# Kernel tuning notes

Hardware: AMD Instinct MI355X
Metric: run time of the kernel (lower is better)

Reference implementation:

```python
import jax, jax.numpy as jnp
import numpy as np

N = 100000
E = 3200000
B = 8192
IN_DIM = 18   # enc_dim for khops=2
HID = 64
EMB = 32


def setup_inputs() -> dict:
    key = jax.random.key(0)
    ks = jax.random.split(key, 10)
    x = jax.random.normal(ks[0], (N, IN_DIM), dtype=jnp.float32)
    ei = jax.random.randint(ks[1], (2, E), 0, N, dtype=jnp.int64)
    targets = jax.random.randint(ks[2], (2, B), 0, N, dtype=jnp.int64)
    # GCN layer params (glorot-ish scale)
    W1 = jax.random.normal(ks[3], (IN_DIM, HID), dtype=jnp.float32) / np.sqrt(IN_DIM)
    b1 = jnp.zeros((HID,), dtype=jnp.float32)
    W2 = jax.random.normal(ks[4], (HID, EMB), dtype=jnp.float32) / np.sqrt(HID)
    b2 = jnp.zeros((EMB,), dtype=jnp.float32)
    Wo = jax.random.normal(ks[5], (EMB, 1), dtype=jnp.float32) / np.sqrt(EMB)
    bo = jnp.zeros((1,), dtype=jnp.float32)
    return {"x": x, "ei": ei, "targets": targets,
            "W1": W1, "b1": b1, "W2": W2, "b2": b2, "Wo": Wo, "bo": bo}


def _gcn_conv(x, W, b, src, dst, norm, n_nodes):
    # x' = D^{-1/2}(A+I)D^{-1/2} X W + b  (self-loops already in src/dst)
    h = x @ W                                  # [N, F_out]
    msg = h[src] * norm[:, None]               # [E+N, F_out] gather
    agg = jax.ops.segment_sum(msg, dst, num_segments=n_nodes)  # scatter-add
    return agg + b


def reference(x, ei, targets, W1, b1, W2, b2, Wo, bo):
    n = x.shape[0]
    loop = jnp.arange(n, dtype=ei.dtype)
    src = jnp.concatenate([ei[0], loop])
    dst = jnp.concatenate([ei[1], loop])
    deg = jax.ops.segment_sum(jnp.ones_like(src, dtype=x.dtype), dst, num_segments=n)
    dis = jax.lax.rsqrt(deg)                   # deg >= 1 (self-loops)
    norm = dis[src] * dis[dst]
    # 2-layer GCN (khops=2): relu between layers, dropout=0 (eval)
    h = jax.nn.relu(_gcn_conv(x, W1, b1, src, dst, norm, n))
    z = _gcn_conv(h, W2, b2, src, dst, norm, n)
    # node-pair multiply + linear head
    pair = z[targets[0]] * z[targets[1]]       # [B, EMB]
    return pair @ Wo + bo                      # [B, 1]
```

## Files before the change

### kernel.cpp

```cpp
#include <hip/hip_runtime.h>

#define IN_DIM 18
#define XPAD 20
#define HID 64
#define EMB 32
#define NGROUP 8
#define PSHIFT 9
#define PMAX 200
#define BCAP 40
#define TILE 4096
#define SCAP 16896

typedef int vint4 __attribute__((ext_vector_type(4)));
typedef unsigned long long u64;

__device__ inline float4 shfl_f4(float4 v, int srcLane) {
    float4 r;
    r.x = __shfl(v.x, srcLane);
    r.y = __shfl(v.y, srcLane);
    r.z = __shfl(v.z, srcLane);
    r.w = __shfl(v.w, srcLane);
    return r;
}

__device__ inline float4 shfl_xor_f4(float4 v, int m) {
    v.x = __shfl_xor(v.x, m);
    v.y = __shfl_xor(v.y, m);
    v.z = __shfl_xor(v.z, m);
    v.w = __shfl_xor(v.w, m);
    return v;
}


__global__ void k_init(int* __restrict__ deg, int* __restrict__ gcnt, int n) {
    int i = blockIdx.x * 256 + threadIdx.x;
    if (i < n) deg[i] = 1;
    if (i < 256) gcnt[i] = 0;
}


__global__ void k_part(const int* __restrict__ src, const int* __restrict__ dst,
                       int* __restrict__ gcnt, u64* __restrict__ gbuf,
                       int e, int Pp, int cap) {
    __shared__ u64 sbuf[PMAX][BCAP];
    __shared__ int scnt[PMAX];
    __shared__ int sbase[PMAX];
    int tid = threadIdx.x;
    int ntile = (e + TILE - 1) / TILE;
    for (int tile = blockIdx.x; tile < ntile; tile += gridDim.x) {
        for (int p = tid; p < Pp; p += 256) scnt[p] = 0;
        __syncthreads();
#pragma unroll
        for (int r = 0; r < TILE / 1024; ++r) {
            int i = tile * TILE + (r * 256 + tid) * 4;
            if (i + 4 <= e) {
                vint4 s4 = __builtin_nontemporal_load((const vint4*)(src + i));
                vint4 d4 = __builtin_nontemporal_load((const vint4*)(dst + i));
#pragma unroll
                for (int k = 0; k < 4; ++k) {
                    int d = d4[k];
                    int p = d >> PSHIFT;
                    u64 pr = ((u64)(unsigned)s4[k] << 32) | (unsigned)d;
                    int pos = atomicAdd(&scnt[p], 1);
                    if (pos < BCAP) sbuf[p][pos] = pr;
                    else {
                        int gp = atomicAdd(&gcnt[p], 1);
                        __builtin_nontemporal_store(pr, &gbuf[(size_t)p * cap + gp]);
                    }
                }
            } else if (i < e) {
                for (int k = i; k < e; ++k) {
                    int d = dst[k];
                    int p = d >> PSHIFT;
                    u64 pr = ((u64)(unsigned)src[k] << 32) | (unsigned)d;
                    int pos = atomicAdd(&scnt[p], 1);
                    if (pos < BCAP) sbuf[p][pos] = pr;
                    else {
                        int gp = atomicAdd(&gcnt[p], 1);
                        __builtin_nontemporal_store(pr, &gbuf[(size_t)p * cap + gp]);
                    }
                }
            }
        }
        __syncthreads();
        for (int p = tid; p < Pp; p += 256)
            sbase[p] = atomicAdd(&gcnt[p], min(scnt[p], BCAP));
        __syncthreads();
        int wid = tid >> 6, lane = tid & 63;
        for (int p = wid; p < Pp; p += 4) {
            int c = min(scnt[p], BCAP);
            int b = sbase[p];
            for (int k = lane; k < c; k += 64)
                __builtin_nontemporal_store(sbuf[p][k], &gbuf[(size_t)p * cap + b + k]);
        }
        __syncthreads();
    }
}


__global__ void k_gscan(const int* __restrict__ gcnt, int* __restrict__ gbase, int Pp) {
    __shared__ int s[256];
    int t = threadIdx.x;
    int v = (t < Pp) ? gcnt[t] : 0;
    s[t] = v;
    __syncthreads();
    for (int off = 1; off < 256; off <<= 1) {
        int u = (t >= off) ? s[t - off] : 0;
        __syncthreads();
        s[t] += u;
        __syncthreads();
    }
    if (t < Pp) gbase[t] = s[t] - v;
}


__global__ void k_build(const u64* __restrict__ gbuf, const int* __restrict__ gcnt,
                        const int* __restrict__ gbase, int* __restrict__ deg,
                        float* __restrict__ dis, int* __restrict__ row_ptr,
                        int* __restrict__ adj, int cap, int n) {
    __shared__ u64 spairs[SCAP];
    __shared__ int sdeg[512];
    __shared__ int sexcl[512];
    __shared__ int swp[512];
    __shared__ int sscan[512];
    int p = blockIdx.x;
    int tid = threadIdx.x;
    int lo = p << PSHIFT;
    int nn = min(n - lo, 512);
    int cnt = gcnt[p];
    int base = gbase[p];
    const u64* buf = gbuf + (size_t)p * cap;

    sdeg[tid] = 0;
    int scap = min(cnt, SCAP);
    for (int k = tid; k < scap; k += 512)
        spairs[k] = __builtin_nontemporal_load(&buf[k]);
    __syncthreads();
    for (int k = tid; k < cnt; k += 512) {
        u64 pr = (k < SCAP) ? spairs[k] : __builtin_nontemporal_load(&buf[k]);
        atomicAdd(&sdeg[(int)(pr & 0xffffffffu) - lo], 1);
    }
    __syncthreads();
    int v = sdeg[tid];
    sscan[tid] = v;
    __syncthreads();
    for (int off = 1; off < 512; off <<= 1) {
        int u = (tid >= off) ? sscan[tid - off] : 0;
        __syncthreads();
        sscan[tid] += u;
        __syncthreads();
    }
    sexcl[tid] = sscan[tid] - v;
    swp[tid] = 0;
    __syncthreads();
    if (tid < nn) {
        int dg = sdeg[tid] + 1;
        deg[lo + tid] = dg;
        dis[lo + tid] = rsqrtf((float)dg);
        row_ptr[lo + tid] = base + sexcl[tid];
    }
    for (int k = tid; k < cnt; k += 512) {
        u64 pr = (k < SCAP) ? spairs[k] : __builtin_nontemporal_load(&buf[k]);
        int dl = (int)(pr & 0xffffffffu) - lo;
        int slot = sexcl[dl] + atomicAdd(&swp[dl], 1);
        adj[base + slot] = (int)(pr >> 32);
    }
}


__global__ void k_count_part(const int* __restrict__ dst, int* __restrict__ deg,
                             int e, int nrange, int n) {
    int g  = blockIdx.x & (NGROUP - 1);
    int lo = g * nrange;
    int hi = min(n, lo + nrange);
    int bid  = blockIdx.x >> 3;
    int nblk = gridDim.x >> 3;
    int i0   = (bid * 256 + threadIdx.x) * 4;
    int step = nblk * 256 * 4;
    for (int i = i0; i < e; i += step) {
        if (i + 4 <= e) {
            int4 d4 = *(const int4*)(dst + i);
            if (d4.x >= lo && d4.x < hi) atomicAdd(&deg[d4.x], 1);
            if (d4.y >= lo && d4.y < hi) atomicAdd(&deg[d4.y], 1);
            if (d4.z >= lo && d4.z < hi) atomicAdd(&deg[d4.z], 1);
            if (d4.w >= lo && d4.w < hi) atomicAdd(&deg[d4.w], 1);
        } else {
            for (int k = i; k < e; ++k) {
                int d = dst[k];
                if (d >= lo && d < hi) atomicAdd(&deg[d], 1);
            }
        }
    }
}

__global__ void k_dis(const int* __restrict__ deg, float* __restrict__ dis, int n) {
    int i = blockIdx.x * 256 + threadIdx.x;
    if (i < n) dis[i] = rsqrtf((float)deg[i]);
}

__global__ void k_scanA(const int* __restrict__ deg, int* __restrict__ row_ptr,
                        int* __restrict__ blksums, int n) {
    __shared__ int s[1024];
    int tid = threadIdx.x;
    int i = blockIdx.x * 1024 + tid;
    int v = (i < n) ? (deg[i] - 1) : 0;
    s[tid] = v;
    __syncthreads();
    for (int off = 1; off < 1024; off <<= 1) {
        int t = (tid >= off) ? s[tid - off] : 0;
        __syncthreads();
        s[tid] += t;
        __syncthreads();
    }
    if (i < n) row_ptr[i] = s[tid] - v;
    if (tid == 1023) blksums[blockIdx.x] = s[1023];
}

__global__ void k_scanB(const int* __restrict__ blksums, int* __restrict__ blkoffs, int nb) {
    __shared__ int s[1024];
    int tid = threadIdx.x;
    int v = (tid < nb) ? blksums[tid] : 0;
    s[tid] = v;
    __syncthreads();
    for (int off = 1; off < 1024; off <<= 1) {
        int t = (tid >= off) ? s[tid - off] : 0;
        __syncthreads();
        s[tid] += t;
        __syncthreads();
    }
    if (tid < nb) blkoffs[tid] = s[tid] - v;
}

__global__ void k_scanC(int* __restrict__ row_ptr, const int* __restrict__ blkoffs,
                        int* __restrict__ write_ptr, int n) {
    int i = blockIdx.x * 1024 + threadIdx.x;
    if (i < n) {
        int r = row_ptr[i] + blkoffs[blockIdx.x];
        row_ptr[i] = r;
        write_ptr[i] = r;
    }
}

__global__ void k_fill_part(const int* __restrict__ src, const int* __restrict__ dst,
                            int* __restrict__ write_ptr, int* __restrict__ adj,
                            int e, int nrange, int n) {
    int g  = blockIdx.x & (NGROUP - 1);
    int lo = g * nrange;
    int hi = min(n, lo + nrange);
    int bid  = blockIdx.x >> 3;
    int nblk = gridDim.x >> 3;
    int i0   = (bid * 256 + threadIdx.x) * 4;
    int step = nblk * 256 * 4;
    for (int i = i0; i < e; i += step) {
        if (i + 4 <= e) {
            int4 d4 = *(const int4*)(dst + i);
            if (d4.x >= lo && d4.x < hi) { int slot = atomicAdd(&write_ptr[d4.x], 1); adj[slot] = src[i];     }
            if (d4.y >= lo && d4.y < hi) { int slot = atomicAdd(&write_ptr[d4.y], 1); adj[slot] = src[i + 1]; }
            if (d4.z >= lo && d4.z < hi) { int slot = atomicAdd(&write_ptr[d4.z], 1); adj[slot] = src[i + 2]; }
            if (d4.w >= lo && d4.w < hi) { int slot = atomicAdd(&write_ptr[d4.w], 1); adj[slot] = src[i + 3]; }
        } else {
            for (int k = i; k < e; ++k) {
                int d = dst[k];
                if (d >= lo && d < hi) { int slot = atomicAdd(&write_ptr[d], 1); adj[slot] = src[k]; }
            }
        }
    }
}


__global__ void k_xn(const float* __restrict__ x, const float* __restrict__ dis,
                     float* __restrict__ xn, int n) {
    int gid = blockIdx.x * 256 + threadIdx.x;
    if (gid >= n * 5) return;
    int i = gid / 5, s = gid - (gid / 5) * 5;
    float dn = dis[i];
    const float* xr = x + (size_t)i * IN_DIM;
    float4 v;
    int k = s * 4;
    v.x = (k + 0 < IN_DIM) ? xr[k + 0] * dn : 0.f;
    v.y = (k + 1 < IN_DIM) ? xr[k + 1] * dn : 0.f;
    v.z = (k + 2 < IN_DIM) ? xr[k + 2] * dn : 0.f;
    v.w = (k + 3 < IN_DIM) ? xr[k + 3] * dn : 0.f;
    *(float4*)(xn + (size_t)i * XPAD + k) = v;
}


__global__ void k_agg1f(const float* __restrict__ xn, const int* __restrict__ row_ptr,
                        const int* __restrict__ deg, const int* __restrict__ adj,
                        const float* __restrict__ dis, const float* __restrict__ W1,
                        const float* __restrict__ b1, const float* __restrict__ W2,
                        float* __restrict__ hn2, int n) {
    __shared__ float sw[IN_DIM * HID];
    __shared__ float sw2[HID * EMB];
    __shared__ float sb[HID];
    __shared__ __align__(16) float sagg[4][XPAD];
    __shared__ float sh[4][HID];
    int tid = threadIdx.x;
    for (int t = tid; t < IN_DIM * HID; t += 256) sw[t] = W1[t];
    for (int t = tid; t < HID * EMB; t += 256) sw2[t] = W2[t];
    if (tid < HID) sb[tid] = b1[tid];
    __syncthreads();
    int node = blockIdx.x * 4 + (tid >> 6);
    if (node >= n) return;
    int lane = tid & 63;
    int wv = tid >> 6;
    int eg = lane / 5;
    int sl = lane - eg * 5;
    bool act = eg < 12;
    int beg = row_ptr[node];
    int cnt = deg[node] - 1;
    const int* a = adj + beg;
    float4 acc = make_float4(0.f, 0.f, 0.f, 0.f);
    int base = 0;
    for (; base + 24 <= cnt; base += 24) {
        if (act) {
            int j0 = a[base + eg];
            int j1 = a[base + 12 + eg];
            float4 v0 = *(const float4*)(xn + (size_t)j0 * XPAD + sl * 4);
            float4 v1 = *(const float4*)(xn + (size_t)j1 * XPAD + sl * 4);
            acc.x += v0.x + v1.x; acc.y += v0.y + v1.y;
            acc.z += v0.z + v1.z; acc.w += v0.w + v1.w;
        }
    }
    if (act && base + eg < cnt) {
        float4 v = *(const float4*)(xn + (size_t)a[base + eg] * XPAD + sl * 4);
        acc.x += v.x; acc.y += v.y; acc.z += v.z; acc.w += v.w;
    }
    if (act && base + 12 + eg < cnt) {
        float4 v = *(const float4*)(xn + (size_t)a[base + 12 + eg] * XPAD + sl * 4);
        acc.x += v.x; acc.y += v.y; acc.z += v.z; acc.w += v.w;
    }
    float4 t = shfl_f4(acc, lane + 30);
    if (lane < 30) { acc.x += t.x; acc.y += t.y; acc.z += t.z; acc.w += t.w; }
    t = shfl_f4(acc, lane + 15);
    if (lane < 15) { acc.x += t.x; acc.y += t.y; acc.z += t.z; acc.w += t.w; }
    t = shfl_f4(acc, lane + 10);
    if (lane < 5) { acc.x += t.x; acc.y += t.y; acc.z += t.z; acc.w += t.w; }
    t = shfl_f4(acc, lane + 5);
    if (lane < 5) { acc.x += t.x; acc.y += t.y; acc.z += t.z; acc.w += t.w; }
    float dn = dis[node];
    if (lane < 5) {
        float4 s4v = *(const float4*)(xn + (size_t)node * XPAD + lane * 4);
        acc.x += s4v.x; acc.y += s4v.y; acc.z += s4v.z; acc.w += s4v.w;
        *(float4*)&sagg[wv][lane * 4] = acc;
    }
    float s = 0.f;
#pragma unroll
    for (int k = 0; k < IN_DIM; ++k) s += sagg[wv][k] * sw[k * HID + lane];
    float hv = dn * s + sb[lane];
    sh[wv][lane] = hv > 0.f ? hv : 0.f;
    int g = lane & 31, half = lane >> 5;
    float s2 = 0.f;
#pragma unroll
    for (int k = 0; k < 32; ++k) s2 += sh[wv][half * 32 + k] * sw2[(half * 32 + k) * EMB + g];
    s2 += __shfl_xor(s2, 32);
    if (half == 0) hn2[(size_t)node * EMB + g] = dn * s2;
}


__global__ void k_agg2(const float* __restrict__ hn2, const int* __restrict__ row_ptr,
                       const int* __restrict__ deg, const int* __restrict__ adj,
                       const float* __restrict__ dis, const float* __restrict__ b2,
                       float* __restrict__ z, int n) {
    int node = blockIdx.x * 4 + (threadIdx.x >> 6);
    if (node >= n) return;
    int lane = threadIdx.x & 63;
    int eg = lane >> 3;
    int d4 = lane & 7;
    int beg = row_ptr[node];
    int cnt = deg[node] - 1;
    const int* a = adj + beg;
    float4 acc = make_float4(0.f, 0.f, 0.f, 0.f);
    int base = 0;
    for (; base + 24 <= cnt; base += 24) {
        int j0 = a[base + eg];
        int j1 = a[base + 8 + eg];
        int j2 = a[base + 16 + eg];
        float4 v0 = *(const float4*)(hn2 + (size_t)j0 * EMB + d4 * 4);
        float4 v1 = *(const float4*)(hn2 + (size_t)j1 * EMB + d4 * 4);
        float4 v2 = *(const float4*)(hn2 + (size_t)j2 * EMB + d4 * 4);
        acc.x += v0.x + v1.x + v2.x; acc.y += v0.y + v1.y + v2.y;
        acc.z += v0.z + v1.z + v2.z; acc.w += v0.w + v1.w + v2.w;
    }
    int kk = base + eg;
    if (kk < cnt) {
        float4 v = *(const float4*)(hn2 + (size_t)a[kk] * EMB + d4 * 4);
        acc.x += v.x; acc.y += v.y; acc.z += v.z; acc.w += v.w;
    }
    kk += 8;
    if (kk < cnt) {
        float4 v = *(const float4*)(hn2 + (size_t)a[kk] * EMB + d4 * 4);
        acc.x += v.x; acc.y += v.y; acc.z += v.z; acc.w += v.w;
    }
    kk += 8;
    if (kk < cnt) {
        float4 v = *(const float4*)(hn2 + (size_t)a[kk] * EMB + d4 * 4);
        acc.x += v.x; acc.y += v.y; acc.z += v.z; acc.w += v.w;
    }
    float4 t = shfl_xor_f4(acc, 8);
    acc.x += t.x; acc.y += t.y; acc.z += t.z; acc.w += t.w;
    t = shfl_xor_f4(acc, 16);
    acc.x += t.x; acc.y += t.y; acc.z += t.z; acc.w += t.w;
    t = shfl_xor_f4(acc, 32);
    acc.x += t.x; acc.y += t.y; acc.z += t.z; acc.w += t.w;
    if (eg == 0) {
        float4 self = *(const float4*)(hn2 + (size_t)node * EMB + d4 * 4);
        float4 bb = *(const float4*)(b2 + d4 * 4);
        float dn = dis[node];
        float4 o;
        o.x = dn * (acc.x + self.x) + bb.x;
        o.y = dn * (acc.y + self.y) + bb.y;
        o.z = dn * (acc.z + self.z) + bb.z;
        o.w = dn * (acc.w + self.w) + bb.w;
        *(float4*)(z + (size_t)node * EMB + d4 * 4) = o;
    }
}


__global__ void k_head(const float* __restrict__ z, const int* __restrict__ tg,
                       const float* __restrict__ Wo, const float* __restrict__ bo,
                       float* __restrict__ out, int btot) {
    int i = blockIdx.x * 256 + threadIdx.x;
    if (i >= btot) return;
    int t0 = tg[i], t1 = tg[btot + i];
    const float* z0 = z + (size_t)t0 * EMB;
    const float* z1 = z + (size_t)t1 * EMB;
    float acc = 0.f;
#pragma unroll
    for (int g = 0; g < EMB; ++g) acc += z0[g] * z1[g] * Wo[g];
    out[i] = acc + bo[0];
}


extern "C" void kernel_launch(void* const* d_in, const int* in_sizes, int n_in,
                              void* d_out, int out_size, void* d_ws, size_t ws_size,
                              hipStream_t stream) {
    const float* x  = (const float*)d_in[0];
    const int*   ei = (const int*)d_in[1];
    const int*   tg = (const int*)d_in[2];
    const float* W1 = (const float*)d_in[3];
    const float* b1 = (const float*)d_in[4];
    const float* W2 = (const float*)d_in[5];
    const float* b2 = (const float*)d_in[6];
    const float* Wo = (const float*)d_in[7];
    const float* bo = (const float*)d_in[8];
    float* out = (float*)d_out;

    int n = in_sizes[0] / IN_DIM;
    int e = in_sizes[1] / 2;
    int b = in_sizes[2] / 2;
    const int* src = ei;
    const int* dst = ei + e;

    char* ws = (char*)d_ws;
    size_t off = 0;
    auto alloc = [&](size_t bytes) -> char* {
        char* p = ws + off;
        off += (bytes + 255) & ~(size_t)255;
        return p;
    };
    int*   deg       = (int*)alloc((size_t)n * 4);
    int*   row_ptr   = (int*)alloc((size_t)n * 4);
    int*   write_ptr = (int*)alloc((size_t)n * 4);
    int*   blksums   = (int*)alloc(1024 * 4);
    int*   blkoffs   = (int*)alloc(1024 * 4);
    float* dis       = (float*)alloc((size_t)n * 4);
    int*   adj       = (int*)alloc((size_t)e * 4);
    float* xn        = (float*)alloc((size_t)n * XPAD * 4);
    float* bufA      = (float*)alloc((size_t)n * EMB * 4);
    float* bufB      = (float*)alloc((size_t)n * EMB * 4);
    int*   gcnt      = (int*)alloc(1024);
    int*   gbase     = (int*)alloc(1024);

    int Pp = (n + 511) >> PSHIFT;
    int meanb = (Pp > 0) ? (e / Pp) : e;
    int cap = meanb + meanb / 16 + 1024;
    size_t bucket_bytes = (size_t)Pp * cap * 8;
    bool use_buckets = (Pp <= PMAX) && ((off + bucket_bytes + 256) <= ws_size);
    u64* gbuf = (u64*)alloc(bucket_bytes);

    int nb1024 = (n + 1023) / 1024;
    int nrange = (n + NGROUP - 1) / NGROUP;

    k_init<<<(n + 255) / 256, 256, 0, stream>>>(deg, gcnt, n);

    if (use_buckets) {
        k_part<<<512, 256, 0, stream>>>(src, dst, gcnt, gbuf, e, Pp, cap);
        k_gscan<<<1, 256, 0, stream>>>(gcnt, gbase, Pp);
        k_build<<<Pp, 512, 0, stream>>>(gbuf, gcnt, gbase, deg, dis, row_ptr, adj, cap, n);
    } else {
        k_count_part<<<2048, 256, 0, stream>>>(dst, deg, e, nrange, n);
        k_dis<<<(n + 255) / 256, 256, 0, stream>>>(deg, dis, n);
        k_scanA<<<nb1024, 1024, 0, stream>>>(deg, row_ptr, blksums, n);
        k_scanB<<<1, 1024, 0, stream>>>(blksums, blkoffs, nb1024);
        k_scanC<<<nb1024, 1024, 0, stream>>>(row_ptr, blkoffs, write_ptr, n);
        k_fill_part<<<2048, 256, 0, stream>>>(src, dst, write_ptr, adj, e, nrange, n);
    }

    k_xn<<<((size_t)n * 5 + 255) / 256, 256, 0, stream>>>(x, dis, xn, n);
    k_agg1f<<<(n + 3) / 4, 256, 0, stream>>>(xn, row_ptr, deg, adj, dis, W1, b1, W2, bufA, n);
    k_agg2<<<(n + 3) / 4, 256, 0, stream>>>(bufA, row_ptr, deg, adj, dis, b2, bufB, n);

    k_head<<<(b + 255) / 256, 256, 0, stream>>>(bufB, tg, Wo, bo, out, b);
}
```

Baseline: 239.2 us.

## Partition adjacency by source-node range and aggregate in three cache-friendly passes

The CSR build now sorts each node's neighbor list into three sub-ranges by source-id third and records their split points (m1, m2, mend). Each GCN aggregation layer then runs as three passes, each gathering only from one third of the feature table, so the gathered working set is more likely to stay in L2/LLC. Partial sums go through an intermediate buffer. The build also stops staging pairs in shared memory. The trade-off is extra kernel launches, repeated reads of adjacency metadata, and read-modify-write traffic on the partial-sum buffers.

```diff
diff --git a/kernel.cpp b/kernel.cpp
--- a/kernel.cpp
+++ b/kernel.cpp
@@ -9,7 +9,6 @@
 #define PMAX 200
 #define BCAP 40
 #define TILE 4096
-#define SCAP 16896
 
 typedef int vint4 __attribute__((ext_vector_type(4)));
 typedef unsigned long long u64;
@@ -114,14 +113,15 @@
 }
 
 
-__global__ void k_build(const u64* __restrict__ gbuf, const int* __restrict__ gcnt,
-                        const int* __restrict__ gbase, int* __restrict__ deg,
-                        float* __restrict__ dis, int* __restrict__ row_ptr,
-                        int* __restrict__ adj, int cap, int n) {
-    __shared__ u64 spairs[SCAP];
-    __shared__ int sdeg[512];
-    __shared__ int sexcl[512];
-    __shared__ int swp[512];
+__global__ void k_build3(const u64* __restrict__ gbuf, const int* __restrict__ gcnt,
+                         const int* __restrict__ gbase, int* __restrict__ deg,
+                         float* __restrict__ dis, int* __restrict__ row_ptr,
+                         int* __restrict__ m1, int* __restrict__ m2,
+                         int* __restrict__ mend, int* __restrict__ adj,
+                         int cap, int n, int c1, int c2) {
+    __shared__ int sdeg[3][512];
+    __shared__ int sstart[3][512];
+    __shared__ int swp[3][512];
     __shared__ int sscan[512];
     int p = blockIdx.x;
     int tid = threadIdx.x;
@@ -131,18 +131,19 @@
     int base = gbase[p];
     const u64* buf = gbuf + (size_t)p * cap;
 
-    sdeg[tid] = 0;
-    int scap = min(cnt, SCAP);
-    for (int k = tid; k < scap; k += 512)
-        spairs[k] = __builtin_nontemporal_load(&buf[k]);
+    sdeg[0][tid] = 0; sdeg[1][tid] = 0; sdeg[2][tid] = 0;
     __syncthreads();
     for (int k = tid; k < cnt; k += 512) {
-        u64 pr = (k < SCAP) ? spairs[k] : __builtin_nontemporal_load(&buf[k]);
-        atomicAdd(&sdeg[(int)(pr & 0xffffffffu) - lo], 1);
-    }
-    __syncthreads();
-    int v = sdeg[tid];
-    sscan[tid] = v;
+        u64 pr = __builtin_nontemporal_load(&buf[k]);
+        int dl = (int)(pr & 0xffffffffu) - lo;
+        int s = (int)(pr >> 32);
+        int c = (s >= c1) + (s >= c2);
+        atomicAdd(&sdeg[c][dl], 1);
+    }
+    __syncthreads();
+    int t0 = sdeg[0][tid], t1 = sdeg[1][tid], t2 = sdeg[2][tid];
+    int tot = t0 + t1 + t2;
+    sscan[tid] = tot;
     __syncthreads();
     for (int off = 1; off < 512; off <<= 1) {
         int u = (tid >= off) ? sscan[tid - off] : 0;
@@ -150,20 +151,28 @@
         sscan[tid] += u;
         __syncthreads();
     }
-    sexcl[tid] = sscan[tid] - v;
-    swp[tid] = 0;
+    int excl = sscan[tid] - tot;
+    sstart[0][tid] = excl;
+    sstart[1][tid] = excl + t0;
+    sstart[2][tid] = excl + t0 + t1;
+    swp[0][tid] = 0; swp[1][tid] = 0; swp[2][tid] = 0;
     __syncthreads();
     if (tid < nn) {
-        int dg = sdeg[tid] + 1;
+        int dg = tot + 1;
         deg[lo + tid] = dg;
         dis[lo + tid] = rsqrtf((float)dg);
-        row_ptr[lo + tid] = base + sexcl[tid];
+        row_ptr[lo + tid] = base + excl;
+        m1[lo + tid]  = base + sstart[1][tid];
+        m2[lo + tid]  = base + sstart[2][tid];
+        mend[lo + tid] = base + excl + tot;
     }
     for (int k = tid; k < cnt; k += 512) {
-        u64 pr = (k < SCAP) ? spairs[k] : __builtin_nontemporal_load(&buf[k]);
+        u64 pr = __builtin_nontemporal_load(&buf[k]);
         int dl = (int)(pr & 0xffffffffu) - lo;
-        int slot = sexcl[dl] + atomicAdd(&swp[dl], 1);
-        adj[base + slot] = (int)(pr >> 32);
+        int s = (int)(pr >> 32);
+        int c = (s >= c1) + (s >= c2);
+        int slot = sstart[c][dl] + atomicAdd(&swp[c][dl], 1);
+        adj[base + slot] = s;
     }
 }
 
@@ -267,6 +276,12 @@
     }
 }
 
+__global__ void k_mend(const int* __restrict__ row_ptr, const int* __restrict__ deg,
+                       int* __restrict__ mend, int n) {
+    int i = blockIdx.x * 256 + threadIdx.x;
+    if (i < n) mend[i] = row_ptr[i] + deg[i] - 1;
+}
+
 
 __global__ void k_xn(const float* __restrict__ x, const float* __restrict__ dis,
                      float* __restrict__ xn, int n) {
@@ -285,30 +300,17 @@
 }
 
 
-__global__ void k_agg1f(const float* __restrict__ xn, const int* __restrict__ row_ptr,
-                        const int* __restrict__ deg, const int* __restrict__ adj,
-                        const float* __restrict__ dis, const float* __restrict__ W1,
-                        const float* __restrict__ b1, const float* __restrict__ W2,
-                        float* __restrict__ hn2, int n) {
-    __shared__ float sw[IN_DIM * HID];
-    __shared__ float sw2[HID * EMB];
-    __shared__ float sb[HID];
-    __shared__ __align__(16) float sagg[4][XPAD];
-    __shared__ float sh[4][HID];
-    int tid = threadIdx.x;
-    for (int t = tid; t < IN_DIM * HID; t += 256) sw[t] = W1[t];
-    for (int t = tid; t < HID * EMB; t += 256) sw2[t] = W2[t];
-    if (tid < HID) sb[tid] = b1[tid];
-    __syncthreads();
-    int node = blockIdx.x * 4 + (tid >> 6);
+__global__ void k_agg1p(const float* __restrict__ xn, const int* __restrict__ adj,
+                        const int* __restrict__ lo, const int* __restrict__ hi,
+                        float* __restrict__ agg, int n, int mode) {
+    int node = blockIdx.x * 4 + (threadIdx.x >> 6);
     if (node >= n) return;
-    int lane = tid & 63;
-    int wv = tid >> 6;
+    int lane = threadIdx.x & 63;
     int eg = lane / 5;
     int sl = lane - eg * 5;
     bool act = eg < 12;
-    int beg = row_ptr[node];
-    int cnt = deg[node] - 1;
+    int beg = lo[node];
+    int cnt = hi[node] - beg;
     const int* a = adj + beg;
     float4 acc = make_float4(0.f, 0.f, 0.f, 0.f);
     int base = 0;
@@ -338,10 +340,76 @@
     if (lane < 5) { acc.x += t.x; acc.y += t.y; acc.z += t.z; acc.w += t.w; }
     t = shfl_f4(acc, lane + 5);
     if (lane < 5) { acc.x += t.x; acc.y += t.y; acc.z += t.z; acc.w += t.w; }
+    if (lane < 5) {
+        float* dp = agg + (size_t)node * XPAD + lane * 4;
+        if (mode) {
+            float4 old = *(float4*)dp;
+            acc.x += old.x; acc.y += old.y; acc.z += old.z; acc.w += old.w;
+        }
+        *(float4*)dp = acc;
+    }
+}
+
+
+__global__ void k_agg1z(const float* __restrict__ xn, const int* __restrict__ adj,
+                        const int* __restrict__ lo, const int* __restrict__ hi,
+                        const float* __restrict__ agg, const float* __restrict__ dis,
+                        const float* __restrict__ W1, const float* __restrict__ b1,
+                        const float* __restrict__ W2, float* __restrict__ hn2, int n) {
+    __shared__ float sw[IN_DIM * HID];
+    __shared__ float sw2[HID * EMB];
+    __shared__ float sb[HID];
+    __shared__ __align__(16) float sagg[4][XPAD];
+    __shared__ float sh[4][HID];
+    int tid = threadIdx.x;
+    for (int t = tid; t < IN_DIM * HID; t += 256) sw[t] = W1[t];
+    for (int t = tid; t < HID * EMB; t += 256) sw2[t] = W2[t];
+    if (tid < HID) sb[tid] = b1[tid];
+    __syncthreads();
+    int node = blockIdx.x * 4 + (tid >> 6);
+    if (node >= n) return;
+    int lane = tid & 63;
+    int wv = tid >> 6;
+    int eg = lane / 5;
+    int sl = lane - eg * 5;
+    bool act = eg < 12;
+    int beg = lo[node];
+    int cnt = hi[node] - beg;
+    const int* a = adj + beg;
+    float4 acc = make_float4(0.f, 0.f, 0.f, 0.f);
+    int base = 0;
+    for (; base + 24 <= cnt; base += 24) {
+        if (act) {
+            int j0 = a[base + eg];
+            int j1 = a[base + 12 + eg];
+            float4 v0 = *(const float4*)(xn + (size_t)j0 * XPAD + sl * 4);
+            float4 v1 = *(const float4*)(xn + (size_t)j1 * XPAD + sl * 4);
+            acc.x += v0.x + v1.x; acc.y += v0.y + v1.y;
+            acc.z += v0.z + v1.z; acc.w += v0.w + v1.w;
+        }
+    }
+    if (act && base + eg < cnt) {
+        float4 v = *(const float4*)(xn + (size_t)a[base + eg] * XPAD + sl * 4);
+        acc.x += v.x; acc.y += v.y; acc.z += v.z; acc.w += v.w;
+    }
+    if (act && base + 12 + eg < cnt) {
+        float4 v = *(const float4*)(xn + (size_t)a[base + 12 + eg] * XPAD + sl * 4);
+        acc.x += v.x; acc.y += v.y; acc.z += v.z; acc.w += v.w;
+    }
+    float4 t = shfl_f4(acc, lane + 30);
+    if (lane < 30) { acc.x += t.x; acc.y += t.y; acc.z += t.z; acc.w += t.w; }
+    t = shfl_f4(acc, lane + 15);
+    if (lane < 15) { acc.x += t.x; acc.y += t.y; acc.z += t.z; acc.w += t.w; }
+    t = shfl_f4(acc, lane + 10);
+    if (lane < 5) { acc.x += t.x; acc.y += t.y; acc.z += t.z; acc.w += t.w; }
+    t = shfl_f4(acc, lane + 5);
+    if (lane < 5) { acc.x += t.x; acc.y += t.y; acc.z += t.z; acc.w += t.w; }
     float dn = dis[node];
     if (lane < 5) {
+        float4 pp = *(const float4*)(agg + (size_t)node * XPAD + lane * 4);
         float4 s4v = *(const float4*)(xn + (size_t)node * XPAD + lane * 4);
-        acc.x += s4v.x; acc.y += s4v.y; acc.z += s4v.z; acc.w += s4v.w;
+        acc.x += pp.x + s4v.x; acc.y += pp.y + s4v.y;
+        acc.z += pp.z + s4v.z; acc.w += pp.w + s4v.w;
         *(float4*)&sagg[wv][lane * 4] = acc;
     }
     float s = 0.f;
@@ -358,17 +426,16 @@
 }
 
 
-__global__ void k_agg2(const float* __restrict__ hn2, const int* __restrict__ row_ptr,
-                       const int* __restrict__ deg, const int* __restrict__ adj,
-                       const float* __restrict__ dis, const float* __restrict__ b2,
-                       float* __restrict__ z, int n) {
+__global__ void k_agg2p(const float* __restrict__ hn2, const int* __restrict__ adj,
+                        const int* __restrict__ lo, const int* __restrict__ hi,
+                        float* __restrict__ z, int n, int mode) {
     int node = blockIdx.x * 4 + (threadIdx.x >> 6);
     if (node >= n) return;
     int lane = threadIdx.x & 63;
     int eg = lane >> 3;
     int d4 = lane & 7;
-    int beg = row_ptr[node];
-    int cnt = deg[node] - 1;
+    int beg = lo[node];
+    int cnt = hi[node] - beg;
     const int* a = adj + beg;
     float4 acc = make_float4(0.f, 0.f, 0.f, 0.f);
     int base = 0;
@@ -404,14 +471,71 @@
     t = shfl_xor_f4(acc, 32);
     acc.x += t.x; acc.y += t.y; acc.z += t.z; acc.w += t.w;
     if (eg == 0) {
+        float* dp = z + (size_t)node * EMB + d4 * 4;
+        if (mode) {
+            float4 old = *(float4*)dp;
+            acc.x += old.x; acc.y += old.y; acc.z += old.z; acc.w += old.w;
+        }
+        *(float4*)dp = acc;
+    }
+}
+
+
+__global__ void k_agg2z(const float* __restrict__ hn2, const int* __restrict__ adj,
+                        const int* __restrict__ lo, const int* __restrict__ hi,
+                        const float* __restrict__ dis, const float* __restrict__ b2,
+                        float* __restrict__ z, int n) {
+    int node = blockIdx.x * 4 + (threadIdx.x >> 6);
+    if (node >= n) return;
+    int lane = threadIdx.x & 63;
+    int eg = lane >> 3;
+    int d4 = lane & 7;
+    int beg = lo[node];
+    int cnt = hi[node] - beg;
+    const int* a = adj + beg;
+    float4 acc = make_float4(0.f, 0.f, 0.f, 0.f);
+    int base = 0;
+    for (; base + 24 <= cnt; base += 24) {
+        int j0 = a[base + eg];
+        int j1 = a[base + 8 + eg];
+        int j2 = a[base + 16 + eg];
+        float4 v0 = *(const float4*)(hn2 + (size_t)j0 * EMB + d4 * 4);
+        float4 v1 = *(const float4*)(hn2 + (size_t)j1 * EMB + d4 * 4);
+        float4 v2 = *(const float4*)(hn2 + (size_t)j2 * EMB + d4 * 4);
+        acc.x += v0.x + v1.x + v2.x; acc.y += v0.y + v1.y + v2.y;
+        acc.z += v0.z + v1.z + v2.z; acc.w += v0.w + v1.w + v2.w;
+    }
+    int kk = base + eg;
+    if (kk < cnt) {
+        float4 v = *(const float4*)(hn2 + (size_t)a[kk] * EMB + d4 * 4);
+        acc.x += v.x; acc.y += v.y; acc.z += v.z; acc.w += v.w;
+    }
+    kk += 8;
+    if (kk < cnt) {
+        float4 v = *(const float4*)(hn2 + (size_t)a[kk] * EMB + d4 * 4);
+        acc.x += v.x; acc.y += v.y; acc.z += v.z; acc.w += v.w;
+    }
+    kk += 8;
+    if (kk < cnt) {
+        float4 v = *(const float4*)(hn2 + (size_t)a[kk] * EMB + d4 * 4);
+        acc.x += v.x; acc.y += v.y; acc.z += v.z; acc.w += v.w;
+    }
+    float4 t = shfl_xor_f4(acc, 8);
+    acc.x += t.x; acc.y += t.y; acc.z += t.z; acc.w += t.w;
+    t = shfl_xor_f4(acc, 16);
+    acc.x += t.x; acc.y += t.y; acc.z += t.z; acc.w += t.w;
+    t = shfl_xor_f4(acc, 32);
+    acc.x += t.x; acc.y += t.y; acc.z += t.z; acc.w += t.w;
+    if (eg == 0) {
+        float4 part = *(float4*)(z + (size_t)node * EMB + d4 * 4);
         float4 self = *(const float4*)(hn2 + (size_t)node * EMB + d4 * 4);
         float4 bb = *(const float4*)(b2 + d4 * 4);
         float dn = dis[node];
         float4 o;
-        o.x = dn * (acc.x + self.x) + bb.x;
-        o.y = dn * (acc.y + self.y) + bb.y;
-        o.z = dn * (acc.z + self.z) + bb.z;
-        o.w = dn * (acc.w + self.w) + bb.w;
+        o.x = dn * (acc.x + part.x + self.x) + bb.x;
+        o.y = dn * (acc.y + part.y + self.y) + bb.y;
+        o.z = dn * (acc.z + part.z + self.z) + bb.z;
+        o.w = dn * (acc.w + part.w + self.w) + bb.w;
         *(float4*)(z + (size_t)node * EMB + d4 * 4) = o;
     }
 }
@@ -462,11 +586,15 @@
     int*   deg       = (int*)alloc((size_t)n * 4);
     int*   row_ptr   = (int*)alloc((size_t)n * 4);
     int*   write_ptr = (int*)alloc((size_t)n * 4);
+    int*   m1        = (int*)alloc((size_t)n * 4);
+    int*   m2        = (int*)alloc((size_t)n * 4);
+    int*   mend      = (int*)alloc((size_t)n * 4);
     int*   blksums   = (int*)alloc(1024 * 4);
     int*   blkoffs   = (int*)alloc(1024 * 4);
     float* dis       = (float*)alloc((size_t)n * 4);
     int*   adj       = (int*)alloc((size_t)e * 4);
     float* xn        = (float*)alloc((size_t)n * XPAD * 4);
+    float* agg       = (float*)alloc((size_t)n * XPAD * 4);
     float* bufA      = (float*)alloc((size_t)n * EMB * 4);
     float* bufB      = (float*)alloc((size_t)n * EMB * 4);
     int*   gcnt      = (int*)alloc(1024);
@@ -481,13 +609,17 @@
 
     int nb1024 = (n + 1023) / 1024;
     int nrange = (n + NGROUP - 1) / NGROUP;
+    int c1 = (n + 2) / 3;
+    int c2 = min(2 * c1, n);
+    int nblk4 = (n + 3) / 4;
 
     k_init<<<(n + 255) / 256, 256, 0, stream>>>(deg, gcnt, n);
 
     if (use_buckets) {
         k_part<<<512, 256, 0, stream>>>(src, dst, gcnt, gbuf, e, Pp, cap);
         k_gscan<<<1, 256, 0, stream>>>(gcnt, gbase, Pp);
-        k_build<<<Pp, 512, 0, stream>>>(gbuf, gcnt, gbase, deg, dis, row_ptr, adj, cap, n);
+        k_build3<<<Pp, 512, 0, stream>>>(gbuf, gcnt, gbase, deg, dis, row_ptr,
+                                         m1, m2, mend, adj, cap, n, c1, c2);
     } else {
         k_count_part<<<2048, 256, 0, stream>>>(dst, deg, e, nrange, n);
         k_dis<<<(n + 255) / 256, 256, 0, stream>>>(deg, dis, n);
@@ -495,11 +627,24 @@
         k_scanB<<<1, 1024, 0, stream>>>(blksums, blkoffs, nb1024);
         k_scanC<<<nb1024, 1024, 0, stream>>>(row_ptr, blkoffs, write_ptr, n);
         k_fill_part<<<2048, 256, 0, stream>>>(src, dst, write_ptr, adj, e, nrange, n);
+        k_mend<<<(n + 255) / 256, 256, 0, stream>>>(row_ptr, deg, mend, n);
     }
 
     k_xn<<<((size_t)n * 5 + 255) / 256, 256, 0, stream>>>(x, dis, xn, n);
-    k_agg1f<<<(n + 3) / 4, 256, 0, stream>>>(xn, row_ptr, deg, adj, dis, W1, b1, W2, bufA, n);
-    k_agg2<<<(n + 3) / 4, 256, 0, stream>>>(bufA, row_ptr, deg, adj, dis, b2, bufB, n);
+
+    if (use_buckets) {
+        k_agg1p<<<nblk4, 256, 0, stream>>>(xn, adj, row_ptr, m1, agg, n, 0);
+        k_agg1p<<<nblk4, 256, 0, stream>>>(xn, adj, m1, m2, agg, n, 1);
+        k_agg1z<<<nblk4, 256, 0, stream>>>(xn, adj, m2, mend, agg, dis, W1, b1, W2, bufA, n);
+        k_agg2p<<<nblk4, 256, 0, stream>>>(bufA, adj, row_ptr, m1, bufB, n, 0);
+        k_agg2p<<<nblk4, 256, 0, stream>>>(bufA, adj, m1, m2, bufB, n, 1);
+        k_agg2z<<<nblk4, 256, 0, stream>>>(bufA, adj, m2, mend, dis, b2, bufB, n);
+    } else {
+        k_agg1p<<<nblk4, 256, 0, stream>>>(xn, adj, row_ptr, mend, agg, n, 0);
+        k_agg1z<<<nblk4, 256, 0, stream>>>(xn, adj, mend, mend, agg, dis, W1, b1, W2, bufA, n);
+        k_agg2p<<<nblk4, 256, 0, stream>>>(bufA, adj, row_ptr, mend, bufB, n, 0);
+        k_agg2z<<<nblk4, 256, 0, stream>>>(bufA, adj, mend, mend, dis, b2, bufB, n);
+    }
 
     k_head<<<(b + 255) / 256, 256, 0, stream>>>(bufB, tg, Wo, bo, out, b);
 }
```

Result: slower. 360.1 us (+50.5%).

## Pack edge pairs into 32-bit words and amortize weight loads over more nodes

Applied to the files above, without the earlier changes.

Edge (src,dst) pairs in the partition buckets are packed into one 32-bit word (src shifted by 9 bits, low 9 bits local dst) instead of 64-bit. This halves bucket traffic and shared-memory footprint, and the shared staging depth per partition doubles. The fused layer-1 kernel now handles 16 nodes per block instead of 4, so the shared W1/W2 staging is loaded once per 16 nodes. Packing limits node ids to below 2^23, which a new guard enforces by falling back to the other path.

```diff
diff --git a/kernel.cpp b/kernel.cpp
--- a/kernel.cpp
+++ b/kernel.cpp
@@ -7,12 +7,13 @@
 #define NGROUP 8
 #define PSHIFT 9
 #define PMAX 200
-#define BCAP 40
+#define BCAP 80
 #define TILE 4096
 #define SCAP 16896
+#define NPB 16
 
 typedef int vint4 __attribute__((ext_vector_type(4)));
-typedef unsigned long long u64;
+typedef unsigned int u32;
 
 __device__ inline float4 shfl_f4(float4 v, int srcLane) {
     float4 r;
@@ -40,9 +41,9 @@
 
 
 __global__ void k_part(const int* __restrict__ src, const int* __restrict__ dst,
-                       int* __restrict__ gcnt, u64* __restrict__ gbuf,
+                       int* __restrict__ gcnt, u32* __restrict__ gbuf,
                        int e, int Pp, int cap) {
-    __shared__ u64 sbuf[PMAX][BCAP];
+    __shared__ u32 sbuf[PMAX][BCAP];
     __shared__ int scnt[PMAX];
     __shared__ int sbase[PMAX];
     int tid = threadIdx.x;
@@ -60,7 +61,7 @@
                 for (int k = 0; k < 4; ++k) {
                     int d = d4[k];
                     int p = d >> PSHIFT;
-                    u64 pr = ((u64)(unsigned)s4[k] << 32) | (unsigned)d;
+                    u32 pr = ((u32)s4[k] << PSHIFT) | (u32)(d & 511);
                     int pos = atomicAdd(&scnt[p], 1);
                     if (pos < BCAP) sbuf[p][pos] = pr;
                     else {
@@ -72,7 +73,7 @@
                 for (int k = i; k < e; ++k) {
                     int d = dst[k];
                     int p = d >> PSHIFT;
-                    u64 pr = ((u64)(unsigned)src[k] << 32) | (unsigned)d;
+                    u32 pr = ((u32)src[k] << PSHIFT) | (u32)(d & 511);
                     int pos = atomicAdd(&scnt[p], 1);
                     if (pos < BCAP) sbuf[p][pos] = pr;
                     else {
@@ -114,11 +115,11 @@
 }
 
 
-__global__ void k_build(const u64* __restrict__ gbuf, const int* __restrict__ gcnt,
+__global__ void k_build(const u32* __restrict__ gbuf, const int* __restrict__ gcnt,
                         const int* __restrict__ gbase, int* __restrict__ deg,
                         float* __restrict__ dis, int* __restrict__ row_ptr,
                         int* __restrict__ adj, int cap, int n) {
-    __shared__ u64 spairs[SCAP];
+    __shared__ u32 spairs[SCAP];
     __shared__ int sdeg[512];
     __shared__ int sexcl[512];
     __shared__ int swp[512];
@@ -129,7 +130,7 @@
     int nn = min(n - lo, 512);
     int cnt = gcnt[p];
     int base = gbase[p];
-    const u64* buf = gbuf + (size_t)p * cap;
+    const u32* buf = gbuf + (size_t)p * cap;
 
     sdeg[tid] = 0;
     int scap = min(cnt, SCAP);
@@ -137,8 +138,8 @@
         spairs[k] = __builtin_nontemporal_load(&buf[k]);
     __syncthreads();
     for (int k = tid; k < cnt; k += 512) {
-        u64 pr = (k < SCAP) ? spairs[k] : __builtin_nontemporal_load(&buf[k]);
-        atomicAdd(&sdeg[(int)(pr & 0xffffffffu) - lo], 1);
+        u32 pr = (k < SCAP) ? spairs[k] : __builtin_nontemporal_load(&buf[k]);
+        atomicAdd(&sdeg[pr & 511], 1);
     }
     __syncthreads();
     int v = sdeg[tid];
@@ -160,10 +161,10 @@
         row_ptr[lo + tid] = base + sexcl[tid];
     }
     for (int k = tid; k < cnt; k += 512) {
-        u64 pr = (k < SCAP) ? spairs[k] : __builtin_nontemporal_load(&buf[k]);
-        int dl = (int)(pr & 0xffffffffu) - lo;
+        u32 pr = (k < SCAP) ? spairs[k] : __builtin_nontemporal_load(&buf[k]);
+        int dl = pr & 511;
         int slot = sexcl[dl] + atomicAdd(&swp[dl], 1);
-        adj[base + slot] = (int)(pr >> 32);
+        adj[base + slot] = (int)(pr >> PSHIFT);
     }
 }
 
@@ -300,61 +301,65 @@
     for (int t = tid; t < HID * EMB; t += 256) sw2[t] = W2[t];
     if (tid < HID) sb[tid] = b1[tid];
     __syncthreads();
-    int node = blockIdx.x * 4 + (tid >> 6);
-    if (node >= n) return;
     int lane = tid & 63;
     int wv = tid >> 6;
     int eg = lane / 5;
     int sl = lane - eg * 5;
     bool act = eg < 12;
-    int beg = row_ptr[node];
-    int cnt = deg[node] - 1;
-    const int* a = adj + beg;
-    float4 acc = make_float4(0.f, 0.f, 0.f, 0.f);
-    int base = 0;
-    for (; base + 24 <= cnt; base += 24) {
-        if (act) {
-            int j0 = a[base + eg];
-            int j1 = a[base + 12 + eg];
-            float4 v0 = *(const float4*)(xn + (size_t)j0 * XPAD + sl * 4);
-            float4 v1 = *(const float4*)(xn + (size_t)j1 * XPAD + sl * 4);
-            acc.x += v0.x + v1.x; acc.y += v0.y + v1.y;
-            acc.z += v0.z + v1.z; acc.w += v0.w + v1.w;
-        }
-    }
-    if (act && base + eg < cnt) {
-        float4 v = *(const float4*)(xn + (size_t)a[base + eg] * XPAD + sl * 4);
-        acc.x += v.x; acc.y += v.y; acc.z += v.z; acc.w += v.w;
-    }
-    if (act && base + 12 + eg < cnt) {
-        float4 v = *(const float4*)(xn + (size_t)a[base + 12 + eg] * XPAD + sl * 4);
-        acc.x += v.x; acc.y += v.y; acc.z += v.z; acc.w += v.w;
-    }
-    float4 t = shfl_f4(acc, lane + 30);
-    if (lane < 30) { acc.x += t.x; acc.y += t.y; acc.z += t.z; acc.w += t.w; }
-    t = shfl_f4(acc, lane + 15);
-    if (lane < 15) { acc.x += t.x; acc.y += t.y; acc.z += t.z; acc.w += t.w; }
-    t = shfl_f4(acc, lane + 10);
-    if (lane < 5) { acc.x += t.x; acc.y += t.y; acc.z += t.z; acc.w += t.w; }
-    t = shfl_f4(acc, lane + 5);
-    if (lane < 5) { acc.x += t.x; acc.y += t.y; acc.z += t.z; acc.w += t.w; }
-    float dn = dis[node];
-    if (lane < 5) {
-        float4 s4v = *(const float4*)(xn + (size_t)node * XPAD + lane * 4);
-        acc.x += s4v.x; acc.y += s4v.y; acc.z += s4v.z; acc.w += s4v.w;
-        *(float4*)&sagg[wv][lane * 4] = acc;
-    }
-    float s = 0.f;
+
+    for (int nd = wv; nd < NPB; nd += 4) {
+        int node = blockIdx.x * NPB + nd;
+        if (node >= n) break;
+        int beg = row_ptr[node];
+        int cnt = deg[node] - 1;
+        const int* a = adj + beg;
+        float4 acc = make_float4(0.f, 0.f, 0.f, 0.f);
+        int base = 0;
+        for (; base + 24 <= cnt; base += 24) {
+            if (act) {
+                int j0 = a[base + eg];
+                int j1 = a[base + 12 + eg];
+                float4 v0 = *(const float4*)(xn + (size_t)j0 * XPAD + sl * 4);
+                float4 v1 = *(const float4*)(xn + (size_t)j1 * XPAD + sl * 4);
+                acc.x += v0.x + v1.x; acc.y += v0.y + v1.y;
+                acc.z += v0.z + v1.z; acc.w += v0.w + v1.w;
+            }
+        }
+        if (act && base + eg < cnt) {
+            float4 v = *(const float4*)(xn + (size_t)a[base + eg] * XPAD + sl * 4);
+            acc.x += v.x; acc.y += v.y; acc.z += v.z; acc.w += v.w;
+        }
+        if (act && base + 12 + eg < cnt) {
+            float4 v = *(const float4*)(xn + (size_t)a[base + 12 + eg] * XPAD + sl * 4);
+            acc.x += v.x; acc.y += v.y; acc.z += v.z; acc.w += v.w;
+        }
+        float4 t = shfl_f4(acc, lane + 30);
+        if (lane < 30) { acc.x += t.x; acc.y += t.y; acc.z += t.z; acc.w += t.w; }
+        t = shfl_f4(acc, lane + 15);
+        if (lane < 15) { acc.x += t.x; acc.y += t.y; acc.z += t.z; acc.w += t.w; }
+        t = shfl_f4(acc, lane + 10);
+        if (lane < 5) { acc.x += t.x; acc.y += t.y; acc.z += t.z; acc.w += t.w; }
+        t = shfl_f4(acc, lane + 5);
+        if (lane < 5) { acc.x += t.x; acc.y += t.y; acc.z += t.z; acc.w += t.w; }
+        float dn = dis[node];
+        if (lane < 5) {
+            float4 s4v = *(const float4*)(xn + (size_t)node * XPAD + lane * 4);
+            acc.x += s4v.x; acc.y += s4v.y; acc.z += s4v.z; acc.w += s4v.w;
+            *(float4*)&sagg[wv][lane * 4] = acc;
+        }
+        float s = 0.f;
 #pragma unroll
-    for (int k = 0; k < IN_DIM; ++k) s += sagg[wv][k] * sw[k * HID + lane];
-    float hv = dn * s + sb[lane];
-    sh[wv][lane] = hv > 0.f ? hv : 0.f;
-    int g = lane & 31, half = lane >> 5;
-    float s2 = 0.f;
+        for (int k = 0; k < IN_DIM; ++k) s += sagg[wv][k] * sw[k * HID + lane];
+        float hv = dn * s + sb[lane];
+        sh[wv][lane] = hv > 0.f ? hv : 0.f;
+        int g = lane & 31, half = lane >> 5;
+        float s2 = 0.f;
 #pragma unroll
-    for (int k = 0; k < 32; ++k) s2 += sh[wv][half * 32 + k] * sw2[(half * 32 + k) * EMB + g];
-    s2 += __shfl_xor(s2, 32);
-    if (half == 0) hn2[(size_t)node * EMB + g] = dn * s2;
+        for (int k = 0; k < 32; ++k)
+            s2 += sh[wv][half * 32 + k] * sw2[(half * 32 + k) * EMB + g];
+        s2 += __shfl_xor(s2, 32);
+        if (half == 0) hn2[(size_t)node * EMB + g] = dn * s2;
+    }
 }
 
 
@@ -475,9 +480,10 @@
     int Pp = (n + 511) >> PSHIFT;
     int meanb = (Pp > 0) ? (e / Pp) : e;
     int cap = meanb + meanb / 16 + 1024;
-    size_t bucket_bytes = (size_t)Pp * cap * 8;
-    bool use_buckets = (Pp <= PMAX) && ((off + bucket_bytes + 256) <= ws_size);
-    u64* gbuf = (u64*)alloc(bucket_bytes);
+    size_t bucket_bytes = (size_t)Pp * cap * 4;
+    bool use_buckets = (Pp <= PMAX) && (n < (1 << 23)) &&
+                       ((off + bucket_bytes + 256) <= ws_size);
+    u32* gbuf = (u32*)alloc(bucket_bytes);
 
     int nb1024 = (n + 1023) / 1024;
     int nrange = (n + NGROUP - 1) / NGROUP;
@@ -498,7 +504,7 @@
     }
 
     k_xn<<<((size_t)n * 5 + 255) / 256, 256, 0, stream>>>(x, dis, xn, n);
-    k_agg1f<<<(n + 3) / 4, 256, 0, stream>>>(xn, row_ptr, deg, adj, dis, W1, b1, W2, bufA, n);
+    k_agg1f<<<(n + NPB - 1) / NPB, 256, 0, stream>>>(xn, row_ptr, deg, adj, dis, W1, b1, W2, bufA, n);
     k_agg2<<<(n + 3) / 4, 256, 0, stream>>>(bufA, row_ptr, deg, adj, dis, b2, bufB, n);
 
     k_head<<<(b + 255) / 256, 256, 0, stream>>>(bufB, tg, Wo, bo, out, b);
```

New measurement: 233.3 us. -2.5%, faster.
